# Performance work log

Hardware: AMD Instinct MI355X
Metric: run time of the kernel (lower is better)

The kernel has to match this reference:

```python
import jax, jax.numpy as jnp
import numpy as np

HEADS = 8
DIM_HEAD = 64
SCALE = DIM_HEAD ** -0.5


def setup_inputs() -> dict:
    key = jax.random.key(0)
    k1, k2, k3, k4 = jax.random.split(key, 4)
    b, dim, l = 4, 512, 2048
    hidden = HEADS * DIM_HEAD  # 512
    x = jax.random.normal(k1, (b, dim, l), dtype=jnp.float32)
    w_qkv = jax.random.normal(k2, (3 * hidden, dim), dtype=jnp.float32) * (dim ** -0.5)
    w_out = jax.random.normal(k3, (dim, hidden), dtype=jnp.float32) * (hidden ** -0.5)
    b_out = jax.random.normal(k4, (dim,), dtype=jnp.float32) * 0.01
    return {"x": x, "w_qkv": w_qkv, "w_out": w_out, "b_out": b_out}


def reference(x, w_qkv, w_out, b_out):
    b, c, l = x.shape
    h, d = HEADS, DIM_HEAD
    # 1x1 Conv1d == channel matmul: [3*hidden, c] x [b, c, l] -> [b, 3*hidden, l]
    qkv = jnp.einsum('oc,bcl->bol', w_qkv, x)
    q, k, v = jnp.split(qkv, 3, axis=1)
    # 'b (h d) l -> b h d l'
    q = q.reshape(b, h, d, l) * SCALE
    k = k.reshape(b, h, d, l)
    v = v.reshape(b, h, d, l)
    sim = jnp.einsum('bhdi,bhdj->bhij', q, k)          # [b, h, l, l]
    attn = jax.nn.softmax(sim, axis=-1)
    out = jnp.einsum('bhij,bhdj->bhid', attn, v)       # [b, h, l, d]
    # 'b h l d -> b (h d) l'
    out = out.transpose(0, 1, 3, 2).reshape(b, h * d, l)
    return jnp.einsum('oc,bcl->bol', w_out, out) + b_out[None, :, None]
```

## Files before the change

### kernel.cpp

```cpp
#include <hip/hip_runtime.h>

#define L_SEQ 2048
#define KDIM  512

typedef __attribute__((ext_vector_type(8))) short short8v;
typedef __attribute__((ext_vector_type(4))) float f32x4;

static __device__ __forceinline__ short f2b(float f) {
    union { float f; unsigned u; } v; v.f = f;
    unsigned r = v.u + 0x7fffu + ((v.u >> 16) & 1u);
    return (short)(r >> 16);
}

static __device__ __forceinline__ float fast_exp2(float x) {
#if __has_builtin(__builtin_amdgcn_exp2f)
    return __builtin_amdgcn_exp2f(x);
#else
    return exp2f(x);
#endif
}

static __device__ __forceinline__ void gl2lds16(const short* g, short* l) {
    __builtin_amdgcn_global_load_lds(
        (const __attribute__((address_space(1))) unsigned*)g,
        (__attribute__((address_space(3))) unsigned*)l,
        16, 0, 0);
}

__global__ __launch_bounds__(256) void prep(
    const float* __restrict__ wq, const float* __restrict__ wo,
    const float* __restrict__ x,
    short* __restrict__ wqb, short* __restrict__ wob, short* __restrict__ xT)
{
    __shared__ __align__(16) float T[64 * 72];
    const int t = threadIdx.x;
    int bid = blockIdx.x;

    if (bid < 1024) {
        const int i = bid * 256 + t;
        const int NQ = 1536 * 512 / 4;
        float4 v;
        if (i < NQ) v = ((const float4*)wq)[i];
        else        v = ((const float4*)wo)[i - NQ];
        short4 s;
        s.x = f2b(v.x); s.y = f2b(v.y); s.z = f2b(v.z); s.w = f2b(v.w);
        if (i < NQ) ((short4*)wqb)[i] = s;
        else        ((short4*)wob)[i - NQ] = s;
        return;
    }
    bid -= 1024;
    const int l0 = (bid & 31) * 64;
    const int c0 = ((bid >> 5) & 7) * 64;
    const int b  = bid >> 8;

#pragma unroll
    for (int j = 0; j < 4; ++j) {
        const int idx = j * 256 + t;
        const int row = idx >> 4, c4 = idx & 15;
        const float4 v = *(const float4*)&x[((size_t)b * KDIM + c0 + row) * L_SEQ + l0 + c4 * 4];
        *(float4*)&T[row * 72 + c4 * 4] = v;
    }
    __syncthreads();

#pragma unroll
    for (int j = 0; j < 2; ++j) {
        const int idx = j * 256 + t;
        const int l = idx >> 3, ch = idx & 7;
        short8v s;
#pragma unroll
        for (int e = 0; e < 8; ++e)
            s[e] = f2b(T[(ch * 8 + e) * 72 + l]);
        *(short8v*)&xT[((size_t)b * L_SEQ + l0 + l) * KDIM + c0 + ch * 8] = s;
    }
}

template<int EPI>
__global__ __launch_bounds__(256) void gemm_bt(
    const short* __restrict__ Ag, const short* __restrict__ Bbase,
    const float* __restrict__ bias,
    short* __restrict__ Qws, short* __restrict__ Kws, short* __restrict__ Vws,
    float* __restrict__ Cout)
{
    constexpr int TO   = (EPI == 0) ? 128 : 64;
    constexpr int WO   = TO / 2;
    constexpr int NI   = WO / 16;
    constexpr int CA   = TO * 64 * 2 / 1024;
    constexpr int CB   = 16;
    constexpr int CPW  = (CA + CB) / 4;
    constexpr int SMEM = (EPI == 0) ? 34816 : 24576;

    const int bz = blockIdx.z;
    const int o0 = blockIdx.y * TO;
    const int l0 = blockIdx.x * 128;
    const short* Bg = Bbase + (size_t)bz * L_SEQ * KDIM;

    __shared__ __align__(16) char smem[SMEM];
    short* sA = (short*)smem;
    short* sB = (short*)(smem + TO * 64 * 2);

    const int t    = threadIdx.x;
    const int w    = t >> 6;
    const int lane = t & 63;
    const int quad = lane >> 4;
    const int l16  = lane & 15;
    const int wo   = (w & 1) * WO;
    const int wl   = (w >> 1) * 64;

    f32x4 acc[NI][4];
#pragma unroll
    for (int i = 0; i < NI; ++i)
#pragma unroll
        for (int n = 0; n < 4; ++n) acc[i][n] = (f32x4){0,0,0,0};

    const int lrow = lane >> 3;
    const int lcol = (lane & 7) * 8;

    for (int k0 = 0; k0 < KDIM; k0 += 64) {
#pragma unroll
        for (int p = 0; p < CPW; ++p) {
            const int cid = w * CPW + p;
            if (cid < CA) {
                const int row = cid * 8 + lrow;
                gl2lds16(Ag + (size_t)(o0 + row) * KDIM + k0 + lcol, sA + cid * 512);
            } else {
                const int row = (cid - CA) * 8 + lrow;
                gl2lds16(Bg + (size_t)(l0 + row) * KDIM + k0 + lcol, sB + (cid - CA) * 512);
            }
        }
        __syncthreads();

#pragma unroll
        for (int ks = 0; ks < 2; ++ks) {
            short8v af[NI], bf[4];
#pragma unroll
            for (int i = 0; i < NI; ++i)
                af[i] = *(const short8v*)&sA[(wo + i * 16 + l16) * 64 + ks * 32 + quad * 8];
#pragma unroll
            for (int n = 0; n < 4; ++n)
                bf[n] = *(const short8v*)&sB[(wl + n * 16 + l16) * 64 + ks * 32 + quad * 8];
#pragma unroll
            for (int i = 0; i < NI; ++i)
#pragma unroll
                for (int n = 0; n < 4; ++n)
                    acc[i][n] = __builtin_amdgcn_mfma_f32_16x16x32_bf16(af[i], bf[n], acc[i][n], 0, 0, 0);
        }
        __syncthreads();
    }

    if (EPI == 0) {
        const int type  = o0 >> 9;
        const int local = o0 & 511;
        const int bh0   = bz * 8 + (local >> 6);
        const float sc  = (type == 0) ? 0.18033688011112042f : 1.0f;
        short* T = (short*)smem;

        if (type == 2) {
#pragma unroll
            for (int i = 0; i < NI; ++i)
#pragma unroll
                for (int n = 0; n < 4; ++n)
#pragma unroll
                    for (int r = 0; r < 4; ++r)
                        T[(wo + i * 16 + quad * 4 + r) * 136 + wl + n * 16 + l16] =
                            f2b(acc[i][n][r]);
            __syncthreads();
#pragma unroll
            for (int p = 0; p < 8; ++p) {
                const int idx = p * 256 + t;
                const int o = idx >> 4, c = idx & 15;
                const float4 v = *(const float4*)&T[o * 136 + c * 8];
                short* dst = Vws + ((size_t)(bh0 + (o >> 6)) * 64 + (o & 63)) * L_SEQ + l0 + c * 8;
                *(float4*)dst = v;
            }
        } else {
#pragma unroll
            for (int i = 0; i < NI; ++i)
#pragma unroll
                for (int n = 0; n < 4; ++n) {
                    short4 s;
                    s.x = f2b(acc[i][n][0] * sc);
                    s.y = f2b(acc[i][n][1] * sc);
                    s.z = f2b(acc[i][n][2] * sc);
                    s.w = f2b(acc[i][n][3] * sc);
                    *(short4*)&T[(wl + n * 16 + l16) * 136 + wo + i * 16 + quad * 4] = s;
                }
            __syncthreads();
            short* base = (type == 0) ? Qws : Kws;
#pragma unroll
            for (int p = 0; p < 8; ++p) {
                const int idx = p * 256 + t;
                const int l = idx >> 4, c = idx & 15;
                const float4 v = *(const float4*)&T[l * 136 + c * 8];
                short* dst = base + ((size_t)(bh0 + (c >> 3)) * L_SEQ + l0 + l) * 64 + (c & 7) * 8;
                *(float4*)dst = v;
            }
        }
    } else {
        float* Cb = Cout + (size_t)bz * KDIM * L_SEQ;
#pragma unroll
        for (int i = 0; i < NI; ++i) {
            const int o = o0 + wo + i * 16 + quad * 4;
            float bv[4];
#pragma unroll
            for (int r = 0; r < 4; ++r) bv[r] = bias[o + r];
#pragma unroll
            for (int n = 0; n < 4; ++n) {
                const int l = l0 + wl + n * 16 + l16;
#pragma unroll
                for (int r = 0; r < 4; ++r)
                    Cb[(size_t)(o + r) * L_SEQ + l] = acc[i][n][r] + bv[r];
            }
        }
    }
}

__global__ __launch_bounds__(256) void attn_mfma(
    const short* __restrict__ Qws, const short* __restrict__ Kws,
    const short* __restrict__ Vws, short* __restrict__ ao)
{
    const int bh = blockIdx.x & 31;
    const int b  = bh >> 3;
    const int h  = bh & 7;
    const int i0 = (blockIdx.x >> 5) * 128;

    __shared__ __align__(16) char smem[36864];
    short* Kld = (short*)smem;
    short* Vld = (short*)(smem + 9216);
    short* Pld = (short*)(smem + 18432);
    float* Old = (float*)smem;

    const int t    = threadIdx.x;
    const int w    = t >> 6;
    const int lane = t & 63;
    const int quad = lane >> 4;
    const int l16  = lane & 15;

    const short* Qb = Qws + (size_t)bh * L_SEQ * 64;
    const short* Kb = Kws + (size_t)bh * L_SEQ * 64;
    const short* Vb = Vws + (size_t)bh * 64 * L_SEQ;

    short8v qa[2][2];
#pragma unroll
    for (int hh = 0; hh < 2; ++hh) {
        const short* qrow = Qb + (size_t)(i0 + w * 32 + hh * 16 + l16) * 64 + quad * 8;
        qa[hh][0] = *(const short8v*)qrow;
        qa[hh][1] = *(const short8v*)(qrow + 32);
    }

    f32x4 oacc[2][4];
#pragma unroll
    for (int hh = 0; hh < 2; ++hh)
#pragma unroll
        for (int n = 0; n < 4; ++n) oacc[hh][n] = (f32x4){0,0,0,0};
    float rsum[2] = {0.f, 0.f};
    short* Pw = Pld + w * 32 * 72;

    const int r = t >> 2, c = t & 3;

    for (int j0 = 0; j0 < L_SEQ; j0 += 64) {
        {
            const float4 k0 = *(const float4*)(Kb + (size_t)(j0 + r) * 64 + c * 16);
            const float4 k1 = *(const float4*)(Kb + (size_t)(j0 + r) * 64 + c * 16 + 8);
            const float4 v0 = *(const float4*)(Vb + (size_t)r * L_SEQ + j0 + c * 16);
            const float4 v1 = *(const float4*)(Vb + (size_t)r * L_SEQ + j0 + c * 16 + 8);
            *(float4*)&Kld[r * 72 + c * 16]     = k0;
            *(float4*)&Kld[r * 72 + c * 16 + 8] = k1;
            *(float4*)&Vld[r * 72 + c * 16]     = v0;
            *(float4*)&Vld[r * 72 + c * 16 + 8] = v1;
        }
        __syncthreads();

        f32x4 sacc[2][4];
#pragma unroll
        for (int hh = 0; hh < 2; ++hh)
#pragma unroll
            for (int n = 0; n < 4; ++n) sacc[hh][n] = (f32x4){0,0,0,0};
#pragma unroll
        for (int n = 0; n < 4; ++n) {
            short8v kf0 = *(const short8v*)&Kld[(n * 16 + l16) * 72 + quad * 8];
            short8v kf1 = *(const short8v*)&Kld[(n * 16 + l16) * 72 + 32 + quad * 8];
#pragma unroll
            for (int hh = 0; hh < 2; ++hh) {
                sacc[hh][n] = __builtin_amdgcn_mfma_f32_16x16x32_bf16(kf0, qa[hh][0], sacc[hh][n], 0, 0, 0);
                sacc[hh][n] = __builtin_amdgcn_mfma_f32_16x16x32_bf16(kf1, qa[hh][1], sacc[hh][n], 0, 0, 0);
            }
        }

#pragma unroll
        for (int hh = 0; hh < 2; ++hh)
#pragma unroll
            for (int n = 0; n < 4; ++n) {
                const float p0 = fast_exp2(sacc[hh][n][0]);
                const float p1 = fast_exp2(sacc[hh][n][1]);
                const float p2 = fast_exp2(sacc[hh][n][2]);
                const float p3 = fast_exp2(sacc[hh][n][3]);
                rsum[hh] += (p0 + p1) + (p2 + p3);
                uint2 pv;
                pv.x = __builtin_amdgcn_perm(__float_as_uint(p1), __float_as_uint(p0), 0x07060302u);
                pv.y = __builtin_amdgcn_perm(__float_as_uint(p3), __float_as_uint(p2), 0x07060302u);
                *(uint2*)&Pw[(hh * 16 + l16) * 72 + n * 16 + quad * 4] = pv;
            }

        short8v pa[2][2];
#pragma unroll
        for (int hh = 0; hh < 2; ++hh) {
            pa[hh][0] = *(const short8v*)&Pw[(hh * 16 + l16) * 72 + quad * 8];
            pa[hh][1] = *(const short8v*)&Pw[(hh * 16 + l16) * 72 + 32 + quad * 8];
        }
#pragma unroll
        for (int n = 0; n < 4; ++n) {
            short8v vf0 = *(const short8v*)&Vld[(n * 16 + l16) * 72 + quad * 8];
            short8v vf1 = *(const short8v*)&Vld[(n * 16 + l16) * 72 + 32 + quad * 8];
#pragma unroll
            for (int hh = 0; hh < 2; ++hh) {
                oacc[hh][n] = __builtin_amdgcn_mfma_f32_16x16x32_bf16(pa[hh][0], vf0, oacc[hh][n], 0, 0, 0);
                oacc[hh][n] = __builtin_amdgcn_mfma_f32_16x16x32_bf16(pa[hh][1], vf1, oacc[hh][n], 0, 0, 0);
            }
        }
        __syncthreads();
    }

    float inv[2];
#pragma unroll
    for (int hh = 0; hh < 2; ++hh) {
        rsum[hh] += __shfl_xor(rsum[hh], 16, 64);
        rsum[hh] += __shfl_xor(rsum[hh], 32, 64);
        inv[hh] = 1.0014f / rsum[hh];
    }

#pragma unroll
    for (int hh = 0; hh < 2; ++hh)
#pragma unroll
        for (int rr = 0; rr < 4; ++rr) {
            const float iv = __shfl(inv[hh], quad * 4 + rr, 64);
#pragma unroll
            for (int n = 0; n < 4; ++n)
                Old[(w * 32 + hh * 16 + quad * 4 + rr) * 68 + n * 16 + l16] =
                    oacc[hh][n][rr] * iv;
        }
    __syncthreads();
#pragma unroll
    for (int p = 0; p < 8; ++p) {
        const int idx = p * 256 + t;
        const int i = idx >> 4, c4 = idx & 15;
        const float4 v = *(const float4*)&Old[i * 68 + c4 * 4];
        short4 s;
        s.x = f2b(v.x); s.y = f2b(v.y); s.z = f2b(v.z); s.w = f2b(v.w);
        *(short4*)&ao[((size_t)b * L_SEQ + i0 + i) * KDIM + h * 64 + c4 * 4] = s;
    }
}

extern "C" void kernel_launch(void* const* d_in, const int* in_sizes, int n_in,
                              void* d_out, int out_size, void* d_ws, size_t ws_size,
                              hipStream_t stream)
{
    const float* x     = (const float*)d_in[0];
    const float* w_qkv = (const float*)d_in[1];
    const float* w_out = (const float*)d_in[2];
    const float* b_out = (const float*)d_in[3];
    float* out = (float*)d_out;

    char* ws = (char*)d_ws;
    short* xT    = (short*)ws;                      ws += (size_t)4 * L_SEQ * KDIM * 2;
    short* wq_bf = (short*)ws;                      ws += (size_t)1536 * 512 * 2;
    short* wo_bf = (short*)ws;                      ws += (size_t)512 * 512 * 2;
    short* Qws   = (short*)ws;                      ws += (size_t)32 * L_SEQ * 64 * 2;
    short* Kws   = (short*)ws;                      ws += (size_t)32 * L_SEQ * 64 * 2;
    short* Vws   = (short*)ws;                      ws += (size_t)32 * L_SEQ * 64 * 2;
    short* ao    = (short*)ws;

    dim3 blk(256);
    prep       <<<dim3(2048), blk, 0, stream>>>(w_qkv, w_out, x, wq_bf, wo_bf, xT);
    gemm_bt<0> <<<dim3(16, 12, 4), blk, 0, stream>>>(wq_bf, xT, nullptr, Qws, Kws, Vws, nullptr);
    attn_mfma  <<<dim3(512), blk, 0, stream>>>(Qws, Kws, Vws, ao);
    gemm_bt<1> <<<dim3(16, 8, 4), blk, 0, stream>>>(wo_bf, ao, b_out, nullptr, nullptr, nullptr, out);
}
```

Measured before the change: 168.1 us.

## Load K/V fragments directly from global into registers, double-buffer K, drop LDS staging

The attention kernel no longer stages K and V tiles through shared memory. Each wave now loads its MFMA fragments straight from global memory into registers, with K double-buffered one tile ahead, and the per-tile __syncthreads barriers are removed. Only the per-wave P buffer stays in LDS, and one barrier is added before the output staging. This cuts block-wide syncs and LDS traffic, but every wave (four per block) now loads the same K/V fragments redundantly from global/L2, and register pressure rises.

```diff
diff --git a/kernel.cpp b/kernel.cpp
--- a/kernel.cpp
+++ b/kernel.cpp
@@ -214,6 +214,71 @@
     }
 }
 
+static __device__ __forceinline__ void load_ktile(
+    short8v (&ka)[8], const short* __restrict__ kp, const int j0)
+{
+#pragma unroll
+    for (int n = 0; n < 4; ++n) {
+        ka[n * 2]     = *(const short8v*)(kp + (size_t)(j0 + n * 16) * 64);
+        ka[n * 2 + 1] = *(const short8v*)(kp + (size_t)(j0 + n * 16) * 64 + 32);
+    }
+}
+
+static __device__ __forceinline__ void attn_tile(
+    const short8v (&ka)[8], const short* __restrict__ vp, const int j0,
+    const short8v (&qa)[2][2], f32x4 (&oacc)[2][4], float (&rsum)[2],
+    short* __restrict__ Pw, const int l16, const int quad)
+{
+    short8v va[8];
+#pragma unroll
+    for (int n = 0; n < 4; ++n) {
+        va[n * 2]     = *(const short8v*)(vp + (size_t)n * 16 * L_SEQ + j0);
+        va[n * 2 + 1] = *(const short8v*)(vp + (size_t)n * 16 * L_SEQ + j0 + 32);
+    }
+
+    f32x4 sacc[2][4];
+#pragma unroll
+    for (int hh = 0; hh < 2; ++hh)
+#pragma unroll
+        for (int n = 0; n < 4; ++n) sacc[hh][n] = (f32x4){0, 0, 0, 0};
+#pragma unroll
+    for (int n = 0; n < 4; ++n)
+#pragma unroll
+        for (int hh = 0; hh < 2; ++hh) {
+            sacc[hh][n] = __builtin_amdgcn_mfma_f32_16x16x32_bf16(ka[n * 2],     qa[hh][0], sacc[hh][n], 0, 0, 0);
+            sacc[hh][n] = __builtin_amdgcn_mfma_f32_16x16x32_bf16(ka[n * 2 + 1], qa[hh][1], sacc[hh][n], 0, 0, 0);
+        }
+
+#pragma unroll
+    for (int hh = 0; hh < 2; ++hh)
+#pragma unroll
+        for (int n = 0; n < 4; ++n) {
+            const float p0 = fast_exp2(sacc[hh][n][0]);
+            const float p1 = fast_exp2(sacc[hh][n][1]);
+            const float p2 = fast_exp2(sacc[hh][n][2]);
+            const float p3 = fast_exp2(sacc[hh][n][3]);
+            rsum[hh] += (p0 + p1) + (p2 + p3);
+            uint2 pv;
+            pv.x = __builtin_amdgcn_perm(__float_as_uint(p1), __float_as_uint(p0), 0x07060302u);
+            pv.y = __builtin_amdgcn_perm(__float_as_uint(p3), __float_as_uint(p2), 0x07060302u);
+            *(uint2*)&Pw[(hh * 16 + l16) * 72 + n * 16 + quad * 4] = pv;
+        }
+
+    short8v pa[2][2];
+#pragma unroll
+    for (int hh = 0; hh < 2; ++hh) {
+        pa[hh][0] = *(const short8v*)&Pw[(hh * 16 + l16) * 72 + quad * 8];
+        pa[hh][1] = *(const short8v*)&Pw[(hh * 16 + l16) * 72 + 32 + quad * 8];
+    }
+#pragma unroll
+    for (int n = 0; n < 4; ++n)
+#pragma unroll
+        for (int hh = 0; hh < 2; ++hh) {
+            oacc[hh][n] = __builtin_amdgcn_mfma_f32_16x16x32_bf16(pa[hh][0], va[n * 2],     oacc[hh][n], 0, 0, 0);
+            oacc[hh][n] = __builtin_amdgcn_mfma_f32_16x16x32_bf16(pa[hh][1], va[n * 2 + 1], oacc[hh][n], 0, 0, 0);
+        }
+}
+
 __global__ __launch_bounds__(256) void attn_mfma(
     const short* __restrict__ Qws, const short* __restrict__ Kws,
     const short* __restrict__ Vws, short* __restrict__ ao)
@@ -223,10 +288,8 @@
     const int h  = bh & 7;
     const int i0 = (blockIdx.x >> 5) * 128;
 
-    __shared__ __align__(16) char smem[36864];
-    short* Kld = (short*)smem;
-    short* Vld = (short*)(smem + 9216);
-    short* Pld = (short*)(smem + 18432);
+    __shared__ __align__(16) char smem[34816];
+    short* Pld = (short*)smem;
     float* Old = (float*)smem;
 
     const int t    = threadIdx.x;
@@ -251,73 +314,21 @@
 #pragma unroll
     for (int hh = 0; hh < 2; ++hh)
 #pragma unroll
-        for (int n = 0; n < 4; ++n) oacc[hh][n] = (f32x4){0,0,0,0};
+        for (int n = 0; n < 4; ++n) oacc[hh][n] = (f32x4){0, 0, 0, 0};
     float rsum[2] = {0.f, 0.f};
     short* Pw = Pld + w * 32 * 72;
 
-    const int r = t >> 2, c = t & 3;
-
-    for (int j0 = 0; j0 < L_SEQ; j0 += 64) {
-        {
-            const float4 k0 = *(const float4*)(Kb + (size_t)(j0 + r) * 64 + c * 16);
-            const float4 k1 = *(const float4*)(Kb + (size_t)(j0 + r) * 64 + c * 16 + 8);
-            const float4 v0 = *(const float4*)(Vb + (size_t)r * L_SEQ + j0 + c * 16);
-            const float4 v1 = *(const float4*)(Vb + (size_t)r * L_SEQ + j0 + c * 16 + 8);
-            *(float4*)&Kld[r * 72 + c * 16]     = k0;
-            *(float4*)&Kld[r * 72 + c * 16 + 8] = k1;
-            *(float4*)&Vld[r * 72 + c * 16]     = v0;
-            *(float4*)&Vld[r * 72 + c * 16 + 8] = v1;
-        }
-        __syncthreads();
-
-        f32x4 sacc[2][4];
-#pragma unroll
-        for (int hh = 0; hh < 2; ++hh)
-#pragma unroll
-            for (int n = 0; n < 4; ++n) sacc[hh][n] = (f32x4){0,0,0,0};
-#pragma unroll
-        for (int n = 0; n < 4; ++n) {
-            short8v kf0 = *(const short8v*)&Kld[(n * 16 + l16) * 72 + quad * 8];
-            short8v kf1 = *(const short8v*)&Kld[(n * 16 + l16) * 72 + 32 + quad * 8];
-#pragma unroll
-            for (int hh = 0; hh < 2; ++hh) {
-                sacc[hh][n] = __builtin_amdgcn_mfma_f32_16x16x32_bf16(kf0, qa[hh][0], sacc[hh][n], 0, 0, 0);
-                sacc[hh][n] = __builtin_amdgcn_mfma_f32_16x16x32_bf16(kf1, qa[hh][1], sacc[hh][n], 0, 0, 0);
-            }
-        }
-
-#pragma unroll
-        for (int hh = 0; hh < 2; ++hh)
-#pragma unroll
-            for (int n = 0; n < 4; ++n) {
-                const float p0 = fast_exp2(sacc[hh][n][0]);
-                const float p1 = fast_exp2(sacc[hh][n][1]);
-                const float p2 = fast_exp2(sacc[hh][n][2]);
-                const float p3 = fast_exp2(sacc[hh][n][3]);
-                rsum[hh] += (p0 + p1) + (p2 + p3);
-                uint2 pv;
-                pv.x = __builtin_amdgcn_perm(__float_as_uint(p1), __float_as_uint(p0), 0x07060302u);
-                pv.y = __builtin_amdgcn_perm(__float_as_uint(p3), __float_as_uint(p2), 0x07060302u);
-                *(uint2*)&Pw[(hh * 16 + l16) * 72 + n * 16 + quad * 4] = pv;
-            }
-
-        short8v pa[2][2];
-#pragma unroll
-        for (int hh = 0; hh < 2; ++hh) {
-            pa[hh][0] = *(const short8v*)&Pw[(hh * 16 + l16) * 72 + quad * 8];
-            pa[hh][1] = *(const short8v*)&Pw[(hh * 16 + l16) * 72 + 32 + quad * 8];
-        }
-#pragma unroll
-        for (int n = 0; n < 4; ++n) {
-            short8v vf0 = *(const short8v*)&Vld[(n * 16 + l16) * 72 + quad * 8];
-            short8v vf1 = *(const short8v*)&Vld[(n * 16 + l16) * 72 + 32 + quad * 8];
-#pragma unroll
-            for (int hh = 0; hh < 2; ++hh) {
-                oacc[hh][n] = __builtin_amdgcn_mfma_f32_16x16x32_bf16(pa[hh][0], vf0, oacc[hh][n], 0, 0, 0);
-                oacc[hh][n] = __builtin_amdgcn_mfma_f32_16x16x32_bf16(pa[hh][1], vf1, oacc[hh][n], 0, 0, 0);
-            }
-        }
-        __syncthreads();
+    const short* kp = Kb + (size_t)l16 * 64 + quad * 8;
+    const short* vp = Vb + (size_t)l16 * L_SEQ + quad * 8;
+
+    short8v kA[8], kB[8];
+    load_ktile(kA, kp, 0);
+    for (int j0 = 0; j0 < L_SEQ; j0 += 128) {
+        load_ktile(kB, kp, j0 + 64);
+        attn_tile(kA, vp, j0, qa, oacc, rsum, Pw, l16, quad);
+        if (j0 + 128 < L_SEQ)
+            load_ktile(kA, kp, j0 + 128);
+        attn_tile(kB, vp, j0 + 64, qa, oacc, rsum, Pw, l16, quad);
     }
 
     float inv[2];
@@ -327,6 +338,8 @@
         rsum[hh] += __shfl_xor(rsum[hh], 32, 64);
         inv[hh] = 1.0014f / rsum[hh];
     }
+
+    __syncthreads();
 
 #pragma unroll
     for (int hh = 0; hh < 2; ++hh)
```

Result: slower. 234.7 us (+39.6%).

## Double-buffer K/V tiles in LDS with register prefetch of next tile

Applied to the files above, without the earlier changes.

The attention loop now keeps two LDS buffers for K and V tiles. It issues global loads for the next tile into registers before the current tile's MFMA work, then writes them into the alternate buffer afterwards. This removes one barrier per iteration and hides global load latency behind compute. In exchange, shared memory grows from 36 KB to 54 KB, which may lower occupancy, and register pressure rises from the prefetched values.

```diff
diff --git a/kernel.cpp b/kernel.cpp
--- a/kernel.cpp
+++ b/kernel.cpp
@@ -223,10 +223,8 @@
     const int h  = bh & 7;
     const int i0 = (blockIdx.x >> 5) * 128;
 
-    __shared__ __align__(16) char smem[36864];
-    short* Kld = (short*)smem;
-    short* Vld = (short*)(smem + 9216);
-    short* Pld = (short*)(smem + 18432);
+    __shared__ __align__(16) char smem[55296];
+    short* Pld = (short*)(smem + 36864);
     float* Old = (float*)smem;
 
     const int t    = threadIdx.x;
@@ -257,18 +255,38 @@
 
     const int r = t >> 2, c = t & 3;
 
-    for (int j0 = 0; j0 < L_SEQ; j0 += 64) {
-        {
-            const float4 k0 = *(const float4*)(Kb + (size_t)(j0 + r) * 64 + c * 16);
-            const float4 k1 = *(const float4*)(Kb + (size_t)(j0 + r) * 64 + c * 16 + 8);
-            const float4 v0 = *(const float4*)(Vb + (size_t)r * L_SEQ + j0 + c * 16);
-            const float4 v1 = *(const float4*)(Vb + (size_t)r * L_SEQ + j0 + c * 16 + 8);
-            *(float4*)&Kld[r * 72 + c * 16]     = k0;
-            *(float4*)&Kld[r * 72 + c * 16 + 8] = k1;
-            *(float4*)&Vld[r * 72 + c * 16]     = v0;
-            *(float4*)&Vld[r * 72 + c * 16 + 8] = v1;
-        }
-        __syncthreads();
+    {
+        short* K0 = (short*)smem;
+        short* V0 = (short*)(smem + 9216);
+        const short* kg = Kb + (size_t)r * 64 + c * 16;
+        const short* vg = Vb + (size_t)r * L_SEQ + c * 16;
+        const float4 k0 = *(const float4*)kg;
+        const float4 k1 = *(const float4*)(kg + 8);
+        const float4 v0 = *(const float4*)vg;
+        const float4 v1 = *(const float4*)(vg + 8);
+        *(float4*)&K0[r * 72 + c * 16]     = k0;
+        *(float4*)&K0[r * 72 + c * 16 + 8] = k1;
+        *(float4*)&V0[r * 72 + c * 16]     = v0;
+        *(float4*)&V0[r * 72 + c * 16 + 8] = v1;
+    }
+    __syncthreads();
+
+    for (int jt = 0; jt < L_SEQ / 64; ++jt) {
+        const int j0   = jt * 64;
+        const int coff = (jt & 1) * 18432;
+        short* Kc = (short*)(smem + coff);
+        short* Vc = (short*)(smem + coff + 9216);
+        const bool more = (jt + 1 < L_SEQ / 64);
+
+        float4 nk0, nk1, nv0, nv1;
+        if (more) {
+            const short* kg = Kb + (size_t)(j0 + 64 + r) * 64 + c * 16;
+            const short* vg = Vb + (size_t)r * L_SEQ + j0 + 64 + c * 16;
+            nk0 = *(const float4*)kg;
+            nk1 = *(const float4*)(kg + 8);
+            nv0 = *(const float4*)vg;
+            nv1 = *(const float4*)(vg + 8);
+        }
 
         f32x4 sacc[2][4];
 #pragma unroll
@@ -277,8 +295,8 @@
             for (int n = 0; n < 4; ++n) sacc[hh][n] = (f32x4){0,0,0,0};
 #pragma unroll
         for (int n = 0; n < 4; ++n) {
-            short8v kf0 = *(const short8v*)&Kld[(n * 16 + l16) * 72 + quad * 8];
-            short8v kf1 = *(const short8v*)&Kld[(n * 16 + l16) * 72 + 32 + quad * 8];
+            short8v kf0 = *(const short8v*)&Kc[(n * 16 + l16) * 72 + quad * 8];
+            short8v kf1 = *(const short8v*)&Kc[(n * 16 + l16) * 72 + 32 + quad * 8];
 #pragma unroll
             for (int hh = 0; hh < 2; ++hh) {
                 sacc[hh][n] = __builtin_amdgcn_mfma_f32_16x16x32_bf16(kf0, qa[hh][0], sacc[hh][n], 0, 0, 0);
@@ -309,13 +327,23 @@
         }
 #pragma unroll
         for (int n = 0; n < 4; ++n) {
-            short8v vf0 = *(const short8v*)&Vld[(n * 16 + l16) * 72 + quad * 8];
-            short8v vf1 = *(const short8v*)&Vld[(n * 16 + l16) * 72 + 32 + quad * 8];
+            short8v vf0 = *(const short8v*)&Vc[(n * 16 + l16) * 72 + quad * 8];
+            short8v vf1 = *(const short8v*)&Vc[(n * 16 + l16) * 72 + 32 + quad * 8];
 #pragma unroll
             for (int hh = 0; hh < 2; ++hh) {
                 oacc[hh][n] = __builtin_amdgcn_mfma_f32_16x16x32_bf16(pa[hh][0], vf0, oacc[hh][n], 0, 0, 0);
                 oacc[hh][n] = __builtin_amdgcn_mfma_f32_16x16x32_bf16(pa[hh][1], vf1, oacc[hh][n], 0, 0, 0);
             }
+        }
+
+        if (more) {
+            const int noff = ((jt & 1) ^ 1) * 18432;
+            short* Kn = (short*)(smem + noff);
+            short* Vn = (short*)(smem + noff + 9216);
+            *(float4*)&Kn[r * 72 + c * 16]     = nk0;
+            *(float4*)&Kn[r * 72 + c * 16 + 8] = nk1;
+            *(float4*)&Vn[r * 72 + c * 16]     = nv0;
+            *(float4*)&Vn[r * 72 + c * 16 + 8] = nv1;
         }
         __syncthreads();
     }
```

New measurement: 169.5 us. Within noise of the previous version (+0.9%).

## Software-pipeline attention loop with double-buffered K/V and one-tile-ahead QK scores

Applied to the files above, without the earlier changes.

Restructures the attention main loop so K/V tiles are double-buffered in LDS and loaded from global memory two tiles ahead in registers. The QK^T MFMA for the next tile is interleaved with the exp/P-write of the current tile, so matrix and transcendental work overlap. The cost is more LDS (about 54KB instead of 36KB), which may reduce occupancy, plus more live registers for the second score buffer.

```diff
diff --git a/kernel.cpp b/kernel.cpp
--- a/kernel.cpp
+++ b/kernel.cpp
@@ -214,6 +214,77 @@
     }
 }
 
+template<bool STAGE>
+static __device__ __forceinline__ void attn_body(
+    const int T,
+    const short* Kn, const short* Vc, short* Kw, short* Vw,
+    const short* __restrict__ Kb, const short* __restrict__ Vb,
+    short* __restrict__ Pw,
+    const short8v (&qa)[2][2],
+    f32x4 (&SC)[2][4], f32x4 (&SN)[2][4],
+    f32x4 (&oacc)[2][4], float (&rsum)[2],
+    const int r, const int c, const int l16, const int quad)
+{
+    float4 nk0, nk1, nv0, nv1;
+    if (STAGE) {
+        const short* kg = Kb + (size_t)((T + 2) * 64 + r) * 64 + c * 16;
+        const short* vg = Vb + (size_t)r * L_SEQ + (T + 2) * 64 + c * 16;
+        nk0 = *(const float4*)kg;
+        nk1 = *(const float4*)(kg + 8);
+        nv0 = *(const float4*)vg;
+        nv1 = *(const float4*)(vg + 8);
+    }
+
+#pragma unroll
+    for (int n = 0; n < 4; ++n) {
+        const short8v kf0 = *(const short8v*)&Kn[(n * 16 + l16) * 72 + quad * 8];
+        const short8v kf1 = *(const short8v*)&Kn[(n * 16 + l16) * 72 + 32 + quad * 8];
+#pragma unroll
+        for (int hh = 0; hh < 2; ++hh) {
+            f32x4 s0 = __builtin_amdgcn_mfma_f32_16x16x32_bf16(kf0, qa[hh][0], (f32x4){0.f, 0.f, 0.f, 0.f}, 0, 0, 0);
+            SN[hh][n] = __builtin_amdgcn_mfma_f32_16x16x32_bf16(kf1, qa[hh][1], s0, 0, 0, 0);
+        }
+#pragma unroll
+        for (int hh = 0; hh < 2; ++hh) {
+            const float p0 = fast_exp2(SC[hh][n][0]);
+            const float p1 = fast_exp2(SC[hh][n][1]);
+            const float p2 = fast_exp2(SC[hh][n][2]);
+            const float p3 = fast_exp2(SC[hh][n][3]);
+            rsum[hh] += (p0 + p1) + (p2 + p3);
+            uint2 pv;
+            pv.x = __builtin_amdgcn_perm(__float_as_uint(p1), __float_as_uint(p0), 0x07060302u);
+            pv.y = __builtin_amdgcn_perm(__float_as_uint(p3), __float_as_uint(p2), 0x07060302u);
+            *(uint2*)&Pw[(hh * 16 + l16) * 72 + n * 16 + quad * 4] = pv;
+        }
+    }
+
+    short8v pa[2][2];
+#pragma unroll
+    for (int hh = 0; hh < 2; ++hh) {
+        pa[hh][0] = *(const short8v*)&Pw[(hh * 16 + l16) * 72 + quad * 8];
+        pa[hh][1] = *(const short8v*)&Pw[(hh * 16 + l16) * 72 + 32 + quad * 8];
+    }
+#pragma unroll
+    for (int n = 0; n < 4; ++n) {
+        const short8v vf0 = *(const short8v*)&Vc[(n * 16 + l16) * 72 + quad * 8];
+        const short8v vf1 = *(const short8v*)&Vc[(n * 16 + l16) * 72 + 32 + quad * 8];
+#pragma unroll
+        for (int hh = 0; hh < 2; ++hh) {
+            oacc[hh][n] = __builtin_amdgcn_mfma_f32_16x16x32_bf16(pa[hh][0], vf0, oacc[hh][n], 0, 0, 0);
+            oacc[hh][n] = __builtin_amdgcn_mfma_f32_16x16x32_bf16(pa[hh][1], vf1, oacc[hh][n], 0, 0, 0);
+        }
+    }
+
+    __syncthreads();
+    if (STAGE) {
+        *(float4*)&Kw[r * 72 + c * 16]     = nk0;
+        *(float4*)&Kw[r * 72 + c * 16 + 8] = nk1;
+        *(float4*)&Vw[r * 72 + c * 16]     = nv0;
+        *(float4*)&Vw[r * 72 + c * 16 + 8] = nv1;
+    }
+    __syncthreads();
+}
+
 __global__ __launch_bounds__(256) void attn_mfma(
     const short* __restrict__ Qws, const short* __restrict__ Kws,
     const short* __restrict__ Vws, short* __restrict__ ao)
@@ -223,10 +294,12 @@
     const int h  = bh & 7;
     const int i0 = (blockIdx.x >> 5) * 128;
 
-    __shared__ __align__(16) char smem[36864];
-    short* Kld = (short*)smem;
-    short* Vld = (short*)(smem + 9216);
-    short* Pld = (short*)(smem + 18432);
+    __shared__ __align__(16) char smem[55296];
+    short* K0 = (short*)smem;
+    short* V0 = (short*)(smem + 9216);
+    short* K1 = (short*)(smem + 18432);
+    short* V1 = (short*)(smem + 27648);
+    short* Pld = (short*)(smem + 36864);
     float* Old = (float*)smem;
 
     const int t    = threadIdx.x;
@@ -257,50 +330,60 @@
 
     const int r = t >> 2, c = t & 3;
 
-    for (int j0 = 0; j0 < L_SEQ; j0 += 64) {
-        {
-            const float4 k0 = *(const float4*)(Kb + (size_t)(j0 + r) * 64 + c * 16);
-            const float4 k1 = *(const float4*)(Kb + (size_t)(j0 + r) * 64 + c * 16 + 8);
-            const float4 v0 = *(const float4*)(Vb + (size_t)r * L_SEQ + j0 + c * 16);
-            const float4 v1 = *(const float4*)(Vb + (size_t)r * L_SEQ + j0 + c * 16 + 8);
-            *(float4*)&Kld[r * 72 + c * 16]     = k0;
-            *(float4*)&Kld[r * 72 + c * 16 + 8] = k1;
-            *(float4*)&Vld[r * 72 + c * 16]     = v0;
-            *(float4*)&Vld[r * 72 + c * 16 + 8] = v1;
-        }
-        __syncthreads();
-
-        f32x4 sacc[2][4];
-#pragma unroll
-        for (int hh = 0; hh < 2; ++hh)
-#pragma unroll
-            for (int n = 0; n < 4; ++n) sacc[hh][n] = (f32x4){0,0,0,0};
+    {
+        const short* kg0 = Kb + (size_t)r * 64 + c * 16;
+        const short* vg0 = Vb + (size_t)r * L_SEQ + c * 16;
+        const short* kg1 = Kb + (size_t)(64 + r) * 64 + c * 16;
+        const short* vg1 = Vb + (size_t)r * L_SEQ + 64 + c * 16;
+        const float4 a0 = *(const float4*)kg0, a1 = *(const float4*)(kg0 + 8);
+        const float4 a2 = *(const float4*)vg0, a3 = *(const float4*)(vg0 + 8);
+        const float4 b0 = *(const float4*)kg1, b1 = *(const float4*)(kg1 + 8);
+        const float4 b2 = *(const float4*)vg1, b3 = *(const float4*)(vg1 + 8);
+        *(float4*)&K0[r * 72 + c * 16]     = a0;
+        *(float4*)&K0[r * 72 + c * 16 + 8] = a1;
+        *(float4*)&V0[r * 72 + c * 16]     = a2;
+        *(float4*)&V0[r * 72 + c * 16 + 8] = a3;
+        *(float4*)&K1[r * 72 + c * 16]     = b0;
+        *(float4*)&K1[r * 72 + c * 16 + 8] = b1;
+        *(float4*)&V1[r * 72 + c * 16]     = b2;
+        *(float4*)&V1[r * 72 + c * 16 + 8] = b3;
+    }
+    __syncthreads();
+
+    f32x4 sA[2][4], sB[2][4];
+#pragma unroll
+    for (int n = 0; n < 4; ++n) {
+        const short8v kf0 = *(const short8v*)&K0[(n * 16 + l16) * 72 + quad * 8];
+        const short8v kf1 = *(const short8v*)&K0[(n * 16 + l16) * 72 + 32 + quad * 8];
+#pragma unroll
+        for (int hh = 0; hh < 2; ++hh) {
+            f32x4 s0 = __builtin_amdgcn_mfma_f32_16x16x32_bf16(kf0, qa[hh][0], (f32x4){0.f, 0.f, 0.f, 0.f}, 0, 0, 0);
+            sA[hh][n] = __builtin_amdgcn_mfma_f32_16x16x32_bf16(kf1, qa[hh][1], s0, 0, 0, 0);
+        }
+    }
+
+    for (int it = 0; it < 15; ++it) {
+        const int T = it * 2;
+        attn_body<true >(T,     K1, V0, K0, V0, Kb, Vb, Pw, qa, sA, sB, oacc, rsum, r, c, l16, quad);
+        attn_body<true >(T + 1, K0, V1, K1, V1, Kb, Vb, Pw, qa, sB, sA, oacc, rsum, r, c, l16, quad);
+    }
+    attn_body<false>(30, K1, V0, K0, V0, Kb, Vb, Pw, qa, sA, sB, oacc, rsum, r, c, l16, quad);
+
+#pragma unroll
+    for (int hh = 0; hh < 2; ++hh)
 #pragma unroll
         for (int n = 0; n < 4; ++n) {
-            short8v kf0 = *(const short8v*)&Kld[(n * 16 + l16) * 72 + quad * 8];
-            short8v kf1 = *(const short8v*)&Kld[(n * 16 + l16) * 72 + 32 + quad * 8];
-#pragma unroll
-            for (int hh = 0; hh < 2; ++hh) {
-                sacc[hh][n] = __builtin_amdgcn_mfma_f32_16x16x32_bf16(kf0, qa[hh][0], sacc[hh][n], 0, 0, 0);
-                sacc[hh][n] = __builtin_amdgcn_mfma_f32_16x16x32_bf16(kf1, qa[hh][1], sacc[hh][n], 0, 0, 0);
-            }
-        }
-
-#pragma unroll
-        for (int hh = 0; hh < 2; ++hh)
-#pragma unroll
-            for (int n = 0; n < 4; ++n) {
-                const float p0 = fast_exp2(sacc[hh][n][0]);
-                const float p1 = fast_exp2(sacc[hh][n][1]);
-                const float p2 = fast_exp2(sacc[hh][n][2]);
-                const float p3 = fast_exp2(sacc[hh][n][3]);
-                rsum[hh] += (p0 + p1) + (p2 + p3);
-                uint2 pv;
-                pv.x = __builtin_amdgcn_perm(__float_as_uint(p1), __float_as_uint(p0), 0x07060302u);
-                pv.y = __builtin_amdgcn_perm(__float_as_uint(p3), __float_as_uint(p2), 0x07060302u);
-                *(uint2*)&Pw[(hh * 16 + l16) * 72 + n * 16 + quad * 4] = pv;
-            }
-
+            const float p0 = fast_exp2(sB[hh][n][0]);
+            const float p1 = fast_exp2(sB[hh][n][1]);
+            const float p2 = fast_exp2(sB[hh][n][2]);
+            const float p3 = fast_exp2(sB[hh][n][3]);
+            rsum[hh] += (p0 + p1) + (p2 + p3);
+            uint2 pv;
+            pv.x = __builtin_amdgcn_perm(__float_as_uint(p1), __float_as_uint(p0), 0x07060302u);
+            pv.y = __builtin_amdgcn_perm(__float_as_uint(p3), __float_as_uint(p2), 0x07060302u);
+            *(uint2*)&Pw[(hh * 16 + l16) * 72 + n * 16 + quad * 4] = pv;
+        }
+    {
         short8v pa[2][2];
 #pragma unroll
         for (int hh = 0; hh < 2; ++hh) {
@@ -309,15 +392,14 @@
         }
 #pragma unroll
         for (int n = 0; n < 4; ++n) {
-            short8v vf0 = *(const short8v*)&Vld[(n * 16 + l16) * 72 + quad * 8];
-            short8v vf1 = *(const short8v*)&Vld[(n * 16 + l16) * 72 + 32 + quad * 8];
+            const short8v vf0 = *(const short8v*)&V1[(n * 16 + l16) * 72 + quad * 8];
+            const short8v vf1 = *(const short8v*)&V1[(n * 16 + l16) * 72 + 32 + quad * 8];
 #pragma unroll
             for (int hh = 0; hh < 2; ++hh) {
                 oacc[hh][n] = __builtin_amdgcn_mfma_f32_16x16x32_bf16(pa[hh][0], vf0, oacc[hh][n], 0, 0, 0);
                 oacc[hh][n] = __builtin_amdgcn_mfma_f32_16x16x32_bf16(pa[hh][1], vf1, oacc[hh][n], 0, 0, 0);
             }
         }
-        __syncthreads();
     }
 
     float inv[2];
@@ -327,6 +409,8 @@
         rsum[hh] += __shfl_xor(rsum[hh], 32, 64);
         inv[hh] = 1.0014f / rsum[hh];
     }
+
+    __syncthreads();
 
 #pragma unroll
     for (int hh = 0; hh < 2; ++hh)
```

Result: slower. 189.0 us (+12.5%).
